# Kernel tuning notes

Hardware: AMD Instinct MI355X
Metric: run time of the kernel (lower is better)

The kernel has to match this reference:

```python
import jax, jax.numpy as jnp
import numpy as np

N_EMBD = 1024
N_HEAD = 16

def setup_inputs() -> dict:
    key = jax.random.key(0)
    ks = jax.random.split(key, 5)
    s = 0.02
    x = jax.random.normal(ks[0], (4, 2048, N_EMBD), dtype=jnp.float32)
    W_attn = jax.random.normal(ks[1], (N_EMBD, 3 * N_EMBD), dtype=jnp.float32) * s
    b_attn = jnp.zeros((3 * N_EMBD,), dtype=jnp.float32)
    W_proj = jax.random.normal(ks[2], (N_EMBD, N_EMBD), dtype=jnp.float32) * s
    b_proj = jnp.zeros((N_EMBD,), dtype=jnp.float32)
    return {"x": x, "W_attn": W_attn, "b_attn": b_attn, "W_proj": W_proj, "b_proj": b_proj}

def reference(x, W_attn, b_attn, W_proj, b_proj):
    B, T, C = x.shape
    H = N_HEAD
    Dh = C // H
    qkv = x @ W_attn + b_attn                      # [B,T,3C]
    q, k, v = jnp.split(qkv, 3, axis=2)
    # [B,T,C] -> [B,H,T,Dh]
    q = q.reshape(B, T, H, Dh).transpose(0, 2, 1, 3)
    k = k.reshape(B, T, H, Dh).transpose(0, 2, 1, 3)
    v = v.reshape(B, T, H, Dh).transpose(0, 2, 1, 3)
    scale = 1.0 / jnp.sqrt(jnp.asarray(Dh, dtype=x.dtype))
    att = jnp.einsum('bhqd,bhkd->bhqk', q, k) * scale   # [B,H,T,T]
    causal = jnp.tril(jnp.ones((T, T), dtype=bool))
    att = jnp.where(causal[None, None], att, jnp.asarray(-jnp.inf, dtype=att.dtype))
    att = jax.nn.softmax(att, axis=-1)
    out = jnp.einsum('bhqk,bhkd->bhqd', att, v)          # [B,H,T,Dh]
    out = out.transpose(0, 2, 1, 3).reshape(B, T, C)
    return out @ W_proj + b_proj
```

## Files before the change

kernel.cpp:

```cpp
#include <hip/hip_runtime.h>
#include <hip/hip_bf16.h>
#include <cstdint>

typedef unsigned short u16;
typedef __attribute__((ext_vector_type(8))) short bf16x8;
typedef __attribute__((ext_vector_type(4))) float f32x4;

#define AS1 __attribute__((address_space(1)))
#define AS3 __attribute__((address_space(3)))

#define QSCALE_CONST 0.18033688011112042f
#define SMAX_CONST 8.0f

__device__ __forceinline__ u16 f2bf(float f) {
  union { float f; unsigned u; } v; v.f = f;
  unsigned u = v.u;
  return (u16)((u + 0x7fffu + ((u >> 16) & 1u)) >> 16);
}

__device__ __forceinline__ void gload_lds16(const void* g, const void* l) {
  __builtin_amdgcn_global_load_lds(
      (const AS1 unsigned int*)(uintptr_t)g,
      (AS3 unsigned int*)(unsigned int)(uintptr_t)l,
      16, 0, 0);
}

__global__ __launch_bounds__(256) void cast_bf16_kernel(
    const float* __restrict__ in, u16* __restrict__ out, int n) {
  int i = (blockIdx.x * 256 + threadIdx.x) * 4;
  if (i >= n) return;
  float4 f = *(const float4*)(in + i);
  ushort4 o;
  o.x = f2bf(f.x); o.y = f2bf(f.y); o.z = f2bf(f.z); o.w = f2bf(f.w);
  *(ushort4*)(out + i) = o;
}

__global__ __launch_bounds__(256) void transpose_cast_kernel(
    const float* __restrict__ in, u16* __restrict__ outT, int R, int C) {
  __shared__ float tile[32][33];
  const int c0 = blockIdx.x << 5, r0 = blockIdx.y << 5;
  const int x = threadIdx.x & 31, y = threadIdx.x >> 5;
#pragma unroll
  for (int yy = y; yy < 32; yy += 8)
    tile[yy][x] = in[(size_t)(r0 + yy) * C + c0 + x];
  __syncthreads();
#pragma unroll
  for (int yy = y; yy < 32; yy += 8)
    outT[(size_t)(c0 + yy) * R + r0 + x] = f2bf(tile[x][yy]);
}

template <typename OutT>
__global__ __launch_bounds__(512, 2) void gemm1_kernel(
    const u16* __restrict__ A, const u16* __restrict__ Bt,
    const float* __restrict__ bias, OutT* __restrict__ Cmat,
    int M, int N, int K, int qcols) {
  __shared__ __attribute__((aligned(16))) u16 LA[2][2][128 * 32];
  __shared__ __attribute__((aligned(16))) u16 LB[2][2][256 * 32];

  const int nbn = N >> 8;
  const int nwg = (M >> 7) * nbn;
  int bid = blockIdx.x;
  if ((nwg & 7) == 0) {
    int cpx = nwg >> 3;
    bid = (bid & 7) * cpx + (bid >> 3);
  }
  const int bm = bid / nbn, bn = bid % nbn;

  const int tid = threadIdx.x;
  const int lane = tid & 63, wave = tid >> 6;
  const int g = lane >> 4, l15 = lane & 15;
  const int wm = wave >> 2, wn = wave & 3;

  const u16* Abase = A + (size_t)(bm << 7) * K;
  const u16* Bbase = Bt + (size_t)(bn << 8) * K;

  const int rA = tid >> 2;
  const size_t aoff = (size_t)rA * K + (((tid & 3) ^ ((rA >> 1) & 3)) * 8);
  const int rB0 = tid >> 2;
  const size_t boff0 = (size_t)rB0 * K + (((tid & 3) ^ ((rB0 >> 1) & 3)) * 8);
  const int cB1 = 512 + tid, rB1 = cB1 >> 2;
  const size_t boff1 = (size_t)rB1 * K + (((cB1 & 3) ^ ((rB1 >> 1) & 3)) * 8);

  auto stageG = [&](int buf, int s, int kt) {
    const size_t kof = (size_t)kt * 64 + s * 32;
    gload_lds16(Abase + kof + aoff, &LA[buf][s][0] + tid * 8);
    gload_lds16(Bbase + kof + boff0, &LB[buf][s][0] + tid * 8);
    gload_lds16(Bbase + kof + boff1, &LB[buf][s][0] + (512 + tid) * 8);
  };

  f32x4 zero = {0.f, 0.f, 0.f, 0.f};
  f32x4 acc[4][4];
#pragma unroll
  for (int i = 0; i < 4; ++i)
#pragma unroll
    for (int j = 0; j < 4; ++j) acc[i][j] = zero;

  const int NT = K >> 6;

  stageG(0, 0, 0);
  stageG(0, 1, 0);
  asm volatile("s_waitcnt vmcnt(3)" ::: "memory");
  __builtin_amdgcn_s_barrier();
  __builtin_amdgcn_sched_barrier(0);

#pragma unroll 1
  for (int kt = 0; kt < NT; ++kt) {
    const int cbuf = kt & 1, nbuf = cbuf ^ 1;
    const bool more = (kt + 1 < NT);
#pragma unroll
    for (int s = 0; s < 2; ++s) {
      const char* Ab = (const char*)&LA[cbuf][s][0];
      const char* Bb = (const char*)&LB[cbuf][s][0];
      bf16x8 af[4], bfr[4];
#pragma unroll
      for (int i = 0; i < 4; ++i) {
        int ra = wm * 64 + i * 16 + l15;
        af[i] = *(const bf16x8*)(Ab + ra * 64 + ((g ^ ((ra >> 1) & 3)) << 4));
      }
#pragma unroll
      for (int j = 0; j < 4; ++j) {
        int rb = wn * 64 + j * 16 + l15;
        bfr[j] = *(const bf16x8*)(Bb + rb * 64 + ((g ^ ((rb >> 1) & 3)) << 4));
      }
      if (more) stageG(nbuf, s, kt + 1);
      asm volatile("s_waitcnt lgkmcnt(0)" ::: "memory");
      __builtin_amdgcn_sched_barrier(0);
      __builtin_amdgcn_s_setprio(1);
#pragma unroll
      for (int i = 0; i < 4; ++i)
#pragma unroll
        for (int j = 0; j < 4; ++j)
          acc[i][j] = __builtin_amdgcn_mfma_f32_16x16x32_bf16(af[i], bfr[j], acc[i][j], 0, 0, 0);
      __builtin_amdgcn_s_setprio(0);
      if (more)            asm volatile("s_waitcnt vmcnt(3)" ::: "memory");
      else if (s == 0)     asm volatile("s_waitcnt vmcnt(0)" ::: "memory");
      __builtin_amdgcn_s_barrier();
      __builtin_amdgcn_sched_barrier(0);
    }
  }

#pragma unroll
  for (int i = 0; i < 4; ++i) {
    int row0 = (bm << 7) + wm * 64 + i * 16 + g * 4;
#pragma unroll
    for (int j = 0; j < 4; ++j) {
      int col = (bn << 8) + wn * 64 + j * 16 + l15;
      float bv = bias[col];
      const bool qc = col < qcols;
#pragma unroll
      for (int r = 0; r < 4; ++r) {
        float v = acc[i][j][r] + bv;
        if (qc) v *= QSCALE_CONST;
        size_t idx = (size_t)(row0 + r) * N + col;
        if constexpr (sizeof(OutT) == 2)
          ((u16*)Cmat)[idx] = f2bf(v);
        else
          ((float*)Cmat)[idx] = v;
      }
    }
  }
}

__global__ __launch_bounds__(256, 2) void attn_kernel(
    const u16* __restrict__ qkv, u16* __restrict__ aout) {
  __shared__ __attribute__((aligned(16))) char KsB[2][8192];
  __shared__ __attribute__((aligned(16))) char VtB[2][8192];
  __shared__ __attribute__((aligned(16))) char PbB[4][4096];

  const int bh = blockIdx.x;
  const int b = bh >> 4, h = bh & 15;
  const int tid = threadIdx.x, lane = tid & 63, wave = tid >> 6;
  const int g = lane >> 4, l15 = lane & 15;

  const u16* qbase = qkv + (size_t)b * 2048 * 3072 + h * 64;
  const u16* kbase = qbase + 1024;
  const u16* vbase = qbase + 2048;

  const int krow0 = tid >> 3;
  const int ksc = (tid & 7) ^ (krow0 & 7);
  const size_t ksrc0 = (size_t)krow0 * 3072 + ksc * 8;
  const size_t ksrc1 = ksrc0 + (size_t)32 * 3072;
  const int vp_ = tid >> 3, vdh = tid & 7;
  const size_t vsrc = (size_t)(2 * vp_) * 3072 + vdh * 8;
  const int vkc = vp_ >> 2, vofs = (vp_ & 3) << 2;

  char* pb = PbB[wave];
  const f32x4 sinit = {-SMAX_CONST, -SMAX_CONST, -SMAX_CONST, -SMAX_CONST};
  f32x4 zero = {0.f, 0.f, 0.f, 0.f};

#pragma unroll 1
  for (int jj = 0; jj < 2; ++jj) {
    const int j = jj ? (15 - blockIdx.y) : blockIdx.y;
    const int q0 = j << 7;
    const int qrow = q0 + wave * 32;
    const int nt = 2 * j + 2;

    bf16x8 qfA[2], qfB[2];
#pragma unroll
    for (int kf = 0; kf < 2; ++kf) {
      qfA[kf] = *(const bf16x8*)(qbase + (size_t)(qrow + l15) * 3072 + kf * 32 + g * 8);
      qfB[kf] = *(const bf16x8*)(qbase + (size_t)(qrow + 16 + l15) * 3072 + kf * 32 + g * 8);
    }

    float lsumA = 0.f, lsumB = 0.f;
    f32x4 oA[4], oB[4];
#pragma unroll
    for (int d = 0; d < 4; ++d) { oA[d] = zero; oB[d] = zero; }

    gload_lds16(kbase + ksrc0, KsB[0] + wave * 1024);
    gload_lds16(kbase + ksrc1, KsB[0] + 4096 + wave * 1024);
    {
      bf16x8 v0 = *(const bf16x8*)(vbase + vsrc);
      bf16x8 v1 = *(const bf16x8*)(vbase + vsrc + 3072);
      char* vb = VtB[0];
#pragma unroll
      for (int q = 0; q < 8; ++q) {
        int d = vdh * 8 + q;
        int sig = q ^ vdh;
        unsigned pack = (unsigned)(u16)v0[q] | ((unsigned)(u16)v1[q] << 16);
        *(unsigned*)(vb + d * 128 + ((vkc ^ sig) << 4) + vofs) = pack;
      }
    }

    bf16x8 nv0, nv1;
#pragma unroll 1
    for (int t = 0; t < nt; ++t) {
      const int cur = t & 1;
      const int kv0 = t << 6;
      const bool pre = (t + 1 < nt);
      __syncthreads();

      if (pre) {
        const size_t nxt = (size_t)(t + 1) * 196608;
        gload_lds16(kbase + nxt + ksrc0, KsB[cur ^ 1] + wave * 1024);
        gload_lds16(kbase + nxt + ksrc1, KsB[cur ^ 1] + 4096 + wave * 1024);
        nv0 = *(const bf16x8*)(vbase + nxt + vsrc);
        nv1 = *(const bf16x8*)(vbase + nxt + vsrc + 3072);
      }

      if (qrow + 31 >= kv0) {
        const char* ks = KsB[cur];
        f32x4 sA[4], sB[4];
#pragma unroll
        for (int n = 0; n < 4; ++n) { sA[n] = sinit; sB[n] = sinit; }
#pragma unroll
        for (int kf = 0; kf < 2; ++kf)
#pragma unroll
          for (int n = 0; n < 4; ++n) {
            int row = n * 16 + l15;
            bf16x8 kfr = *(const bf16x8*)(ks + row * 128 + (((kf * 4 + g) ^ (row & 7)) << 4));
            sA[n] = __builtin_amdgcn_mfma_f32_16x16x32_bf16(kfr, qfA[kf], sA[n], 0, 0, 0);
            sB[n] = __builtin_amdgcn_mfma_f32_16x16x32_bf16(kfr, qfB[kf], sB[n], 0, 0, 0);
          }

        const int kvb = kv0 + g * 4;
        if (kv0 + 63 > qrow) {
          const int qgA = qrow + l15;
#pragma unroll
          for (int n = 0; n < 4; ++n)
#pragma unroll
            for (int r = 0; r < 4; ++r)
              if (kvb + n * 16 + r > qgA) sA[n][r] = -1e30f;
        }
        if (kv0 + 63 > qrow + 16) {
          const int qgB = qrow + 16 + l15;
#pragma unroll
          for (int n = 0; n < 4; ++n)
#pragma unroll
            for (int r = 0; r < 4; ++r)
              if (kvb + n * 16 + r > qgB) sB[n][r] = -1e30f;
        }

        float rsA = 0.f, rsB = 0.f;
#pragma unroll
        for (int n = 0; n < 4; ++n)
#pragma unroll
          for (int r = 0; r < 4; ++r) {
            float pA = __builtin_amdgcn_exp2f(sA[n][r]);
            float pB = __builtin_amdgcn_exp2f(sB[n][r]);
            sA[n][r] = pA; rsA += pA;
            sB[n][r] = pB; rsB += pB;
          }
        lsumA += rsA; lsumB += rsB;

#pragma unroll
        for (int n = 0; n < 4; ++n) {
          uint2 wA, wB;
          asm("v_cvt_pk_bf16_f32 %0, %1, %2" : "=v"(wA.x) : "v"(sA[n][0]), "v"(sA[n][1]));
          asm("v_cvt_pk_bf16_f32 %0, %1, %2" : "=v"(wA.y) : "v"(sA[n][2]), "v"(sA[n][3]));
          asm("v_cvt_pk_bf16_f32 %0, %1, %2" : "=v"(wB.x) : "v"(sB[n][0]), "v"(sB[n][1]));
          asm("v_cvt_pk_bf16_f32 %0, %1, %2" : "=v"(wB.y) : "v"(sB[n][2]), "v"(sB[n][3]));
          int c = n * 2 + (g >> 1);
          int boff = (((c ^ (l15 & 7)) << 4) | ((g & 1) << 3)) + l15 * 128;
          *(uint2*)(pb + boff) = wA;
          *(uint2*)(pb + 2048 + boff) = wB;
        }

        const char* vt = VtB[cur];
        bf16x8 pfA[2], pfB[2];
#pragma unroll
        for (int kf = 0; kf < 2; ++kf) {
          int poff = l15 * 128 + (((kf * 4 + g) ^ (l15 & 7)) << 4);
          pfA[kf] = *(const bf16x8*)(pb + poff);
          pfB[kf] = *(const bf16x8*)(pb + 2048 + poff);
        }
#pragma unroll
        for (int kf = 0; kf < 2; ++kf)
#pragma unroll
          for (int d = 0; d < 4; ++d) {
            int dr = d * 16 + l15;
            int sig = (dr & 7) ^ ((dr >> 3) & 7);
            bf16x8 vf = *(const bf16x8*)(vt + dr * 128 + (((kf * 4 + g) ^ sig) << 4));
            oA[d] = __builtin_amdgcn_mfma_f32_16x16x32_bf16(pfA[kf], vf, oA[d], 0, 0, 0);
            oB[d] = __builtin_amdgcn_mfma_f32_16x16x32_bf16(pfB[kf], vf, oB[d], 0, 0, 0);
          }
      }

      if (pre) {
        char* vb = VtB[cur ^ 1];
#pragma unroll
        for (int q = 0; q < 8; ++q) {
          int d = vdh * 8 + q;
          int sig = q ^ vdh;
          unsigned pack = (unsigned)(u16)nv0[q] | ((unsigned)(u16)nv1[q] << 16);
          *(unsigned*)(vb + d * 128 + ((vkc ^ sig) << 4) + vofs) = pack;
        }
      }
    }

    lsumA += __shfl_xor(lsumA, 16); lsumA += __shfl_xor(lsumA, 32);
    lsumB += __shfl_xor(lsumB, 16); lsumB += __shfl_xor(lsumB, 32);
    float invA[4], invB[4];
#pragma unroll
    for (int r = 0; r < 4; ++r) {
      invA[r] = __builtin_amdgcn_rcpf(__shfl(lsumA, g * 4 + r));
      invB[r] = __builtin_amdgcn_rcpf(__shfl(lsumB, g * 4 + r));
    }
    const size_t obase = (size_t)(b * 2048 + qrow) * 1024 + h * 64;
#pragma unroll
    for (int d = 0; d < 4; ++d)
#pragma unroll
      for (int r = 0; r < 4; ++r) {
        aout[obase + (size_t)(g * 4 + r) * 1024 + d * 16 + l15] = f2bf(oA[d][r] * invA[r]);
        aout[obase + (size_t)(16 + g * 4 + r) * 1024 + d * 16 + l15] = f2bf(oB[d][r] * invB[r]);
      }
  }
}

extern "C" void kernel_launch(void* const* d_in, const int* in_sizes, int n_in,
                              void* d_out, int out_size, void* d_ws, size_t ws_size,
                              hipStream_t stream) {
  const float* x      = (const float*)d_in[0];
  const float* W_attn = (const float*)d_in[1];
  const float* b_attn = (const float*)d_in[2];
  const float* W_proj = (const float*)d_in[3];
  const float* b_proj = (const float*)d_in[4];
  float* out = (float*)d_out;

  char* ws = (char*)d_ws;
  u16* xb   = (u16*)(ws);
  u16* Wat  = (u16*)(ws + (size_t)16 * 1024 * 1024);
  u16* Wpt  = (u16*)(ws + (size_t)22 * 1024 * 1024);
  u16* qkv  = (u16*)(ws + (size_t)24 * 1024 * 1024);
  u16* aout = (u16*)(ws + (size_t)72 * 1024 * 1024);

  cast_bf16_kernel<<<8192, 256, 0, stream>>>(x, xb, 8388608);
  transpose_cast_kernel<<<dim3(96, 32), 256, 0, stream>>>(W_attn, Wat, 1024, 3072);
  transpose_cast_kernel<<<dim3(32, 32), 256, 0, stream>>>(W_proj, Wpt, 1024, 1024);
  gemm1_kernel<u16><<<768, 512, 0, stream>>>(xb, Wat, b_attn, qkv, 8192, 3072, 1024, 1024);
  attn_kernel<<<dim3(64, 8), 256, 0, stream>>>(qkv, aout);
  gemm1_kernel<float><<<256, 512, 0, stream>>>(aout, Wpt, b_proj, out, 8192, 1024, 1024, 0);
}
```

Before: 172.6 us.

## Restructure GEMM to 4 waves each owning full 128-row by 64-col subtile

The GEMM workgroup goes from 512 threads (8 waves in a 2x4 grid) to 256 threads (4 waves), with each wave now computing 128x64 of output using 32 accumulators. Each k-tile's global-to-LDS staging is issued as one batch at the top of the iteration, and the hand-tuned waitcnt, setprio and sched_barrier pipelining is replaced with plain __syncthreads. Per-wave register pressure doubles and occupancy falls to one block per CU, which may expose memory latency that the explicit scheduling used to hide.

Result: slower. 178.7 us (+3.5%).

```diff
diff --git a/kernel.cpp b/kernel.cpp
--- a/kernel.cpp
+++ b/kernel.cpp
@@ -50,7 +50,7 @@
 }
 
 template <typename OutT>
-__global__ __launch_bounds__(512, 2) void gemm1_kernel(
+__global__ __launch_bounds__(256, 1) void gemm1_kernel(
     const u16* __restrict__ A, const u16* __restrict__ Bt,
     const float* __restrict__ bias, OutT* __restrict__ Cmat,
     int M, int N, int K, int qcols) {
@@ -69,82 +69,86 @@
   const int tid = threadIdx.x;
   const int lane = tid & 63, wave = tid >> 6;
   const int g = lane >> 4, l15 = lane & 15;
-  const int wm = wave >> 2, wn = wave & 3;
 
   const u16* Abase = A + (size_t)(bm << 7) * K;
   const u16* Bbase = Bt + (size_t)(bn << 8) * K;
 
-  const int rA = tid >> 2;
-  const size_t aoff = (size_t)rA * K + (((tid & 3) ^ ((rA >> 1) & 3)) * 8);
-  const int rB0 = tid >> 2;
-  const size_t boff0 = (size_t)rB0 * K + (((tid & 3) ^ ((rB0 >> 1) & 3)) * 8);
-  const int cB1 = 512 + tid, rB1 = cB1 >> 2;
-  const size_t boff1 = (size_t)rB1 * K + (((cB1 & 3) ^ ((rB1 >> 1) & 3)) * 8);
-
-  auto stageG = [&](int buf, int s, int kt) {
-    const size_t kof = (size_t)kt * 64 + s * 32;
-    gload_lds16(Abase + kof + aoff, &LA[buf][s][0] + tid * 8);
-    gload_lds16(Bbase + kof + boff0, &LB[buf][s][0] + tid * 8);
-    gload_lds16(Bbase + kof + boff1, &LB[buf][s][0] + (512 + tid) * 8);
+  int arow[2], brow[4];
+  size_t aoff[2], boff[4];
+#pragma unroll
+  for (int p = 0; p < 2; ++p) {
+    int c = p * 256 + tid;
+    arow[p] = c >> 2;
+    aoff[p] = (size_t)arow[p] * K + (((c & 3) ^ ((arow[p] >> 1) & 3)) * 8);
+  }
+#pragma unroll
+  for (int p = 0; p < 4; ++p) {
+    int c = p * 256 + tid;
+    brow[p] = c >> 2;
+    boff[p] = (size_t)brow[p] * K + (((c & 3) ^ ((brow[p] >> 1) & 3)) * 8);
+  }
+
+  auto stage = [&](int buf, int kt) {
+    const size_t k0 = (size_t)kt * 64;
+#pragma unroll
+    for (int s = 0; s < 2; ++s) {
+      const size_t kof = k0 + s * 32;
+#pragma unroll
+      for (int p = 0; p < 2; ++p)
+        gload_lds16(Abase + kof + aoff[p], &LA[buf][s][0] + (p * 256 + tid) * 8);
+#pragma unroll
+      for (int p = 0; p < 4; ++p)
+        gload_lds16(Bbase + kof + boff[p], &LB[buf][s][0] + (p * 256 + tid) * 8);
+    }
   };
 
   f32x4 zero = {0.f, 0.f, 0.f, 0.f};
-  f32x4 acc[4][4];
-#pragma unroll
-  for (int i = 0; i < 4; ++i)
+  f32x4 acc[8][4];
+#pragma unroll
+  for (int i = 0; i < 8; ++i)
 #pragma unroll
     for (int j = 0; j < 4; ++j) acc[i][j] = zero;
 
   const int NT = K >> 6;
 
-  stageG(0, 0, 0);
-  stageG(0, 1, 0);
-  asm volatile("s_waitcnt vmcnt(3)" ::: "memory");
-  __builtin_amdgcn_s_barrier();
-  __builtin_amdgcn_sched_barrier(0);
+  stage(0, 0);
+  __syncthreads();
 
 #pragma unroll 1
   for (int kt = 0; kt < NT; ++kt) {
-    const int cbuf = kt & 1, nbuf = cbuf ^ 1;
-    const bool more = (kt + 1 < NT);
+    const int cbuf = kt & 1;
+    if (kt + 1 < NT) stage(cbuf ^ 1, kt + 1);
+
 #pragma unroll
     for (int s = 0; s < 2; ++s) {
       const char* Ab = (const char*)&LA[cbuf][s][0];
       const char* Bb = (const char*)&LB[cbuf][s][0];
-      bf16x8 af[4], bfr[4];
-#pragma unroll
-      for (int i = 0; i < 4; ++i) {
-        int ra = wm * 64 + i * 16 + l15;
+      bf16x8 af[8], bfr[4];
+#pragma unroll
+      for (int j = 0; j < 4; ++j) {
+        int rb = wave * 64 + j * 16 + l15;
+        bfr[j] = *(const bf16x8*)(Bb + rb * 64 + ((g ^ ((rb >> 1) & 3)) << 4));
+      }
+#pragma unroll
+      for (int i = 0; i < 8; ++i) {
+        int ra = i * 16 + l15;
         af[i] = *(const bf16x8*)(Ab + ra * 64 + ((g ^ ((ra >> 1) & 3)) << 4));
       }
 #pragma unroll
-      for (int j = 0; j < 4; ++j) {
-        int rb = wn * 64 + j * 16 + l15;
-        bfr[j] = *(const bf16x8*)(Bb + rb * 64 + ((g ^ ((rb >> 1) & 3)) << 4));
-      }
-      if (more) stageG(nbuf, s, kt + 1);
-      asm volatile("s_waitcnt lgkmcnt(0)" ::: "memory");
-      __builtin_amdgcn_sched_barrier(0);
-      __builtin_amdgcn_s_setprio(1);
-#pragma unroll
-      for (int i = 0; i < 4; ++i)
+      for (int i = 0; i < 8; ++i)
 #pragma unroll
         for (int j = 0; j < 4; ++j)
           acc[i][j] = __builtin_amdgcn_mfma_f32_16x16x32_bf16(af[i], bfr[j], acc[i][j], 0, 0, 0);
-      __builtin_amdgcn_s_setprio(0);
-      if (more)            asm volatile("s_waitcnt vmcnt(3)" ::: "memory");
-      else if (s == 0)     asm volatile("s_waitcnt vmcnt(0)" ::: "memory");
-      __builtin_amdgcn_s_barrier();
-      __builtin_amdgcn_sched_barrier(0);
-    }
-  }
-
-#pragma unroll
-  for (int i = 0; i < 4; ++i) {
-    int row0 = (bm << 7) + wm * 64 + i * 16 + g * 4;
+    }
+    __syncthreads();
+  }
+
+#pragma unroll
+  for (int i = 0; i < 8; ++i) {
+    int row0 = (bm << 7) + i * 16 + g * 4;
 #pragma unroll
     for (int j = 0; j < 4; ++j) {
-      int col = (bn << 8) + wn * 64 + j * 16 + l15;
+      int col = (bn << 8) + wave * 64 + j * 16 + l15;
       float bv = bias[col];
       const bool qc = col < qcols;
 #pragma unroll
@@ -367,7 +371,7 @@
   cast_bf16_kernel<<<8192, 256, 0, stream>>>(x, xb, 8388608);
   transpose_cast_kernel<<<dim3(96, 32), 256, 0, stream>>>(W_attn, Wat, 1024, 3072);
   transpose_cast_kernel<<<dim3(32, 32), 256, 0, stream>>>(W_proj, Wpt, 1024, 1024);
-  gemm1_kernel<u16><<<768, 512, 0, stream>>>(xb, Wat, b_attn, qkv, 8192, 3072, 1024, 1024);
+  gemm1_kernel<u16><<<768, 256, 0, stream>>>(xb, Wat, b_attn, qkv, 8192, 3072, 1024, 1024);
   attn_kernel<<<dim3(64, 8), 256, 0, stream>>>(qkv, aout);
-  gemm1_kernel<float><<<256, 512, 0, stream>>>(aout, Wpt, b_proj, out, 8192, 1024, 1024, 0);
-}
+  gemm1_kernel<float><<<256, 256, 0, stream>>>(aout, Wpt, b_proj, out, 8192, 1024, 1024, 0);
+}
```
